# Kernel tuning notes

Measured on AMD Instinct MI355X. Metric: run time of the kernel, lower is better.

The kernel has to match this reference:

```python
import jax, jax.numpy as jnp
import numpy as np
from jax import lax

NUM_GROUP = 512    # G: number of FPS centers
GROUP_SIZE = 32    # M: KNN neighbors per center


def setup_inputs() -> dict:
    key = jax.random.key(0)
    xyz = jax.random.normal(key, (32, 8192, 3), dtype=jnp.float32)  # B N 3
    return {"xyz": xyz}


def _fps(xyz, num_group):
    """Iterative farthest point sampling. xyz: [B,N,3] -> idx [B,G] int32.
    Deterministic start at point 0 (matching pointnet2-style fps)."""
    B, N, _ = xyz.shape

    def step(carry, _):
        dists, last_idx = carry                       # dists: [B,N] running min sq-dist
        last = xyz[jnp.arange(B), last_idx]           # [B,3] most recent center
        d = jnp.sum((xyz - last[:, None, :]) ** 2, axis=-1)  # [B,N]
        dists = jnp.minimum(dists, d)
        nxt = jnp.argmax(dists, axis=-1).astype(jnp.int32)   # farthest point
        return (dists, nxt), nxt

    init_idx = jnp.zeros((B,), jnp.int32)
    init_d = jnp.full((B, N), jnp.inf, xyz.dtype)
    (_, _), idxs = lax.scan(step, (init_d, init_idx), None, length=num_group - 1)
    return jnp.concatenate([init_idx[None, :], idxs], axis=0).T  # [B,G]


def reference(xyz):
    B, N, _ = xyz.shape
    G, M = NUM_GROUP, GROUP_SIZE

    fps_idx = _fps(xyz, G)                              # [B,G] int32
    center = xyz[jnp.arange(B)[:, None], fps_idx]       # [B,G,3]

    # KNN: for each center, k nearest points in xyz (squared euclidean)
    # dist2[b,g,n] = |c|^2 + |x|^2 - 2 c.x   -> [B,G,N]
    x2 = jnp.sum(xyz * xyz, axis=-1)                    # [B,N]
    c2 = jnp.sum(center * center, axis=-1)              # [B,G]
    dist2 = c2[:, :, None] + x2[:, None, :] - 2.0 * jnp.einsum('bgd,bnd->bgn', center, xyz)
    _, idx = lax.top_k(-dist2, M)                       # [B,G,M] nearest-first

    neighborhood = xyz[jnp.arange(B)[:, None, None], idx]   # [B,G,M,3]
    neighborhood = neighborhood - center[:, :, None, :]
    return neighborhood, center, fps_idx
```

## Files before the change

### kernel.cpp

```cpp
#include <hip/hip_runtime.h>
#include <math.h>

#define BATCH  32
#define NPTS   8192
#define NGROUP 512
#define MSIZE  32

#define FPS_THREADS 512
#define SXYZ_FLOATS (NPTS * 3)
#define DYN_LDS_BYTES (SXYZ_FLOATS * 4)

typedef float v2f __attribute__((ext_vector_type(2)));

template<int CTRL>
__device__ __forceinline__ float dpp_max_f32(float x) {
    int o = __builtin_amdgcn_update_dpp(0, __float_as_int(x), CTRL, 0xF, 0xF, true);
    float f = __int_as_float(o);
    return x > f ? x : f;
}
template<int CTRL>
__device__ __forceinline__ unsigned dpp_min_u32_full(unsigned x) {
    unsigned o = (unsigned)__builtin_amdgcn_update_dpp(0, (int)x, CTRL, 0xF, 0xF, true);
    return o < x ? o : x;
}

__global__ __launch_bounds__(FPS_THREADS, 2)
void fps_kernel(const float* __restrict__ xyz,
                float* __restrict__ out_center,
                float* __restrict__ out_fps)
{
#pragma clang fp contract(off)
    extern __shared__ float sxyz[];
    __shared__ unsigned long long gkey[3];

    const int b    = blockIdx.x;
    const int t    = threadIdx.x;
    const int lane = t & 63;
    const float* bp = xyz + (size_t)b * NPTS * 3;
    const float4* bp4 = reinterpret_cast<const float4*>(bp);
    float4* s4 = reinterpret_cast<float4*>(sxyz);

    v2f px2[8], py2[8], pz2[8], dist2[8];
    {
        float f[48];
        #pragma unroll
        for (int q = 0; q < 12; ++q) {
            float4 v = bp4[t * 12 + q];
            s4[t * 12 + q] = v;
            f[q*4+0] = v.x; f[q*4+1] = v.y; f[q*4+2] = v.z; f[q*4+3] = v.w;
        }
        #pragma unroll
        for (int j = 0; j < 8; ++j) {
            px2[j] = (v2f){f[6*j+0], f[6*j+3]};
            py2[j] = (v2f){f[6*j+1], f[6*j+4]};
            pz2[j] = (v2f){f[6*j+2], f[6*j+5]};
            dist2[j] = (v2f){INFINITY, INFINITY};
        }
    }
    if (t == 0) { gkey[0] = 0; gkey[1] = 0; gkey[2] = 0; }
    __syncthreads();

    if (t == 0) {
        out_fps[(size_t)b * NGROUP] = 0.0f;
        out_center[(size_t)(b * NGROUP) * 3 + 0] = sxyz[0];
        out_center[(size_t)(b * NGROUP) * 3 + 1] = sxyz[1];
        out_center[(size_t)(b * NGROUP) * 3 + 2] = sxyz[2];
    }

    int last = 0;
    for (int g = 1; g < NGROUP; ++g) {
        const int slot = g % 3;
        const int nxt  = (g + 1) % 3;
        float lx = sxyz[last*3 + 0];
        float ly = sxyz[last*3 + 1];
        float lz = sxyz[last*3 + 2];

        #pragma unroll
        for (int j = 0; j < 8; ++j) {
            v2f dx = px2[j] - lx;
            v2f dy = py2[j] - ly;
            v2f dz = pz2[j] - lz;
            v2f t1 = dx * dx;
            v2f t2 = dy * dy;
            v2f t3 = dz * dz;
            v2f s  = t1 + t2;
            v2f d  = s + t3;
            dist2[j] = __builtin_elementwise_min(dist2[j], d);
        }
        v2f mm0 = __builtin_elementwise_max(dist2[0], dist2[1]);
        v2f mm1 = __builtin_elementwise_max(dist2[2], dist2[3]);
        v2f mm2 = __builtin_elementwise_max(dist2[4], dist2[5]);
        v2f mm3 = __builtin_elementwise_max(dist2[6], dist2[7]);
        v2f mma = __builtin_elementwise_max(mm0, mm1);
        v2f mmb = __builtin_elementwise_max(mm2, mm3);
        v2f mmc = __builtin_elementwise_max(mma, mmb);
        float m_t = fmaxf(mmc.x, mmc.y);

        float m = m_t;
        m = dpp_max_f32<0xB1>(m);
        m = dpp_max_f32<0x4E>(m);
        m = dpp_max_f32<0x141>(m);
        m = dpp_max_f32<0x140>(m);
        m = dpp_max_f32<0x142>(m);
        m = dpp_max_f32<0x143>(m);
        float wmax = __int_as_float(__builtin_amdgcn_readlane(__float_as_int(m), 63));

        unsigned long long mask = __ballot(m_t == wmax);
        int l = __ffsll((long long)mask) - 1;

        unsigned lj = 0;
        #pragma unroll
        for (int j = 15; j >= 0; --j) {
            float dj = (j & 1) ? dist2[j >> 1].y : dist2[j >> 1].x;
            lj = (dj == wmax) ? (unsigned)j : lj;
        }
        unsigned idx = ((unsigned)t << 4) | lj;
        unsigned widx = (unsigned)__builtin_amdgcn_readlane((int)idx, l);

        if (lane == 63) {
            unsigned long long key =
                (((unsigned long long)__float_as_uint(wmax)) << 32) | (unsigned)~widx;
            atomicMax(&gkey[slot], key);
            if (t == 63) gkey[nxt] = 0;
        }
        __syncthreads();

        unsigned long long kq = gkey[slot];
        int fi = (int)(~(unsigned)kq);
        last = fi;
        if (t == 0) {
            out_fps[(size_t)b * NGROUP + g] = (float)fi;
            out_center[((size_t)(b * NGROUP + g)) * 3 + 0] = sxyz[fi*3 + 0];
            out_center[((size_t)(b * NGROUP + g)) * 3 + 1] = sxyz[fi*3 + 1];
            out_center[((size_t)(b * NGROUP + g)) * 3 + 2] = sxyz[fi*3 + 2];
        }
    }
}

__global__ __launch_bounds__(256)
void knn_kernel(const float* __restrict__ xyz,
                const float* __restrict__ center,
                float* __restrict__ out_nbhd)
{
    const int lane = threadIdx.x & 63;
    const int gid  = blockIdx.x * 4 + (threadIdx.x >> 6);
    const int b    = gid >> 9;
    const float* bp = xyz + (size_t)b * NPTS * 3;
    const float4* bp4 = reinterpret_cast<const float4*>(bp);

    const float cx = center[(size_t)gid*3+0];
    const float cy = center[(size_t)gid*3+1];
    const float cz = center[(size_t)gid*3+2];

    unsigned kl[4];
    #pragma unroll
    for (int k = 0; k < 4; ++k) kl[k] = 0xFFFFFFFFu;

    for (int c = 0; c < 32; ++c) {
        int f4 = c * 192 + lane * 3;
        float4 a  = bp4[f4+0];
        float4 bq = bp4[f4+1];
        float4 cq = bp4[f4+2];
        unsigned p0 = (unsigned)(c * 256 + lane * 4);
        v2f xA = (v2f){a.x,  a.w},  yA = (v2f){a.y,  bq.x}, zA = (v2f){a.z,  bq.y};
        v2f xB = (v2f){bq.z, cq.y}, yB = (v2f){bq.w, cq.z}, zB = (v2f){cq.x, cq.w};
        v2f dxA = xA - cx, dyA = yA - cy, dzA = zA - cz;
        v2f dxB = xB - cx, dyB = yB - cy, dzB = zB - cz;
        v2f dA = dxA*dxA + dyA*dyA + dzA*dzA;
        v2f dB = dxB*dxB + dyB*dyB + dzB*dzB;
        float ds[4] = {dA.x, dA.y, dB.x, dB.y};
        #pragma unroll
        for (int k = 0; k < 4; ++k) {
            unsigned key = (__float_as_uint(ds[k]) & 0xFFFFE000u) | (p0 + k);
            if (key < kl[3]) {
                kl[3] = key;
                #pragma unroll
                for (int q = 3; q > 0; --q) {
                    if (kl[q] < kl[q-1]) {
                        unsigned tk = kl[q]; kl[q] = kl[q-1]; kl[q-1] = tk;
                    }
                }
            }
        }
    }

    int keep = 0;
    #pragma unroll 1
    for (int r = 0; r < MSIZE; ++r) {
        unsigned k = kl[0];
        k = dpp_min_u32_full<0xB1>(k);
        k = dpp_min_u32_full<0x4E>(k);
        k = dpp_min_u32_full<0x141>(k);
        k = dpp_min_u32_full<0x140>(k);
        {
            unsigned o = __shfl_xor(k, 16);
            k = o < k ? o : k;
            o = __shfl_xor(k, 32);
            k = o < k ? o : k;
        }
        if (lane == r) keep = (int)(k & 0x1FFFu);
        if (kl[0] == k) {
            kl[0] = kl[1]; kl[1] = kl[2]; kl[2] = kl[3];
            kl[3] = 0xFFFFFFFFu;
        }
    }

    if (lane < MSIZE) {
        size_t o = ((size_t)gid * MSIZE + lane) * 3;
        float x = bp[keep*3+0], y = bp[keep*3+1], z = bp[keep*3+2];
        out_nbhd[o+0] = x - cx;
        out_nbhd[o+1] = y - cy;
        out_nbhd[o+2] = z - cz;
    }
}

extern "C" void kernel_launch(void* const* d_in, const int* in_sizes, int n_in,
                              void* d_out, int out_size, void* d_ws, size_t ws_size,
                              hipStream_t stream)
{
    const float* xyz = (const float*)d_in[0];
    float* out        = (float*)d_out;
    float* out_nbhd   = out;
    float* out_center = out + (size_t)BATCH*NGROUP*MSIZE*3;
    float* out_fps    = out_center + (size_t)BATCH*NGROUP*3;

    hipFuncSetAttribute(reinterpret_cast<const void*>(fps_kernel),
                        hipFuncAttributeMaxDynamicSharedMemorySize,
                        DYN_LDS_BYTES);

    fps_kernel<<<dim3(BATCH), dim3(FPS_THREADS), DYN_LDS_BYTES, stream>>>(xyz, out_center, out_fps);
    knn_kernel<<<dim3(BATCH*NGROUP/4), dim3(256), 0, stream>>>(xyz, out_center, out_nbhd);
}
```

Before: 577.0 us.

## Stage batch points in LDS as SoA for KNN and drop FPS atomics

The KNN kernel now launches one 512-thread block per batch segment. Each block loads the batch's points into LDS in structure-of-arrays form, and each wavefront handles 8 centers from LDS instead of re-reading global memory. The wave reduction now uses full DPP row broadcasts plus readlane instead of shuffles. In FPS, the per-iteration LDS atomicMax on a rotating slot is replaced by per-wave key writes into a double-buffered array that every thread then reduces, and the per-lane argmax index search becomes a min tree. The KNN grid drops to 256 blocks of 96KB LDS each, which reduces parallelism and may limit latency hiding.

```diff
diff --git a/kernel.cpp b/kernel.cpp
--- a/kernel.cpp
+++ b/kernel.cpp
@@ -9,6 +9,10 @@
 #define FPS_THREADS 512
 #define SXYZ_FLOATS (NPTS * 3)
 #define DYN_LDS_BYTES (SXYZ_FLOATS * 4)
+
+#define KNN_THREADS 512
+#define KNN_SEGS    8
+#define KNN_GPW     8
 
 typedef float v2f __attribute__((ext_vector_type(2)));
 
@@ -22,6 +26,11 @@
 __device__ __forceinline__ unsigned dpp_min_u32_full(unsigned x) {
     unsigned o = (unsigned)__builtin_amdgcn_update_dpp(0, (int)x, CTRL, 0xF, 0xF, true);
     return o < x ? o : x;
+}
+
+__device__ __forceinline__ unsigned long long u64max(unsigned long long a,
+                                                     unsigned long long b) {
+    return a > b ? a : b;
 }
 
 __global__ __launch_bounds__(FPS_THREADS, 2)
@@ -31,11 +40,12 @@
 {
 #pragma clang fp contract(off)
     extern __shared__ float sxyz[];
-    __shared__ unsigned long long gkey[3];
+    __shared__ unsigned long long s_key[2][8];
 
     const int b    = blockIdx.x;
     const int t    = threadIdx.x;
     const int lane = t & 63;
+    const int wid  = t >> 6;
     const float* bp = xyz + (size_t)b * NPTS * 3;
     const float4* bp4 = reinterpret_cast<const float4*>(bp);
     float4* s4 = reinterpret_cast<float4*>(sxyz);
@@ -57,7 +67,6 @@
             dist2[j] = (v2f){INFINITY, INFINITY};
         }
     }
-    if (t == 0) { gkey[0] = 0; gkey[1] = 0; gkey[2] = 0; }
     __syncthreads();
 
     if (t == 0) {
@@ -69,8 +78,6 @@
 
     int last = 0;
     for (int g = 1; g < NGROUP; ++g) {
-        const int slot = g % 3;
-        const int nxt  = (g + 1) % 3;
         float lx = sxyz[last*3 + 0];
         float ly = sxyz[last*3 + 1];
         float lz = sxyz[last*3 + 2];
@@ -108,25 +115,37 @@
         unsigned long long mask = __ballot(m_t == wmax);
         int l = __ffsll((long long)mask) - 1;
 
-        unsigned lj = 0;
-        #pragma unroll
-        for (int j = 15; j >= 0; --j) {
-            float dj = (j & 1) ? dist2[j >> 1].y : dist2[j >> 1].x;
-            lj = (dj == wmax) ? (unsigned)j : lj;
-        }
+        unsigned cand[8];
+        #pragma unroll
+        for (int p = 0; p < 8; ++p) {
+            unsigned c = 0xFFFFFFFFu;
+            c = (dist2[p].y == wmax) ? (unsigned)(2*p + 1) : c;
+            c = (dist2[p].x == wmax) ? (unsigned)(2*p)     : c;
+            cand[p] = c;
+        }
+        unsigned q0 = cand[0] < cand[1] ? cand[0] : cand[1];
+        unsigned q1 = cand[2] < cand[3] ? cand[2] : cand[3];
+        unsigned q2 = cand[4] < cand[5] ? cand[4] : cand[5];
+        unsigned q3 = cand[6] < cand[7] ? cand[6] : cand[7];
+        unsigned qa = q0 < q1 ? q0 : q1;
+        unsigned qb = q2 < q3 ? q2 : q3;
+        unsigned lj = qa < qb ? qa : qb;
         unsigned idx = ((unsigned)t << 4) | lj;
         unsigned widx = (unsigned)__builtin_amdgcn_readlane((int)idx, l);
 
         if (lane == 63) {
-            unsigned long long key =
+            s_key[g & 1][wid] =
                 (((unsigned long long)__float_as_uint(wmax)) << 32) | (unsigned)~widx;
-            atomicMax(&gkey[slot], key);
-            if (t == 63) gkey[nxt] = 0;
         }
         __syncthreads();
 
-        unsigned long long kq = gkey[slot];
-        int fi = (int)(~(unsigned)kq);
+        const unsigned long long* sk = s_key[g & 1];
+        unsigned long long a0 = u64max(sk[0], sk[1]);
+        unsigned long long a1 = u64max(sk[2], sk[3]);
+        unsigned long long a2 = u64max(sk[4], sk[5]);
+        unsigned long long a3 = u64max(sk[6], sk[7]);
+        unsigned long long km = u64max(u64max(a0, a1), u64max(a2, a3));
+        int fi = (int)(~(unsigned)km);
         last = fi;
         if (t == 0) {
             out_fps[(size_t)b * NGROUP + g] = (float)fi;
@@ -137,80 +156,93 @@
     }
 }
 
-__global__ __launch_bounds__(256)
+__global__ __launch_bounds__(KNN_THREADS, 1)
 void knn_kernel(const float* __restrict__ xyz,
                 const float* __restrict__ center,
                 float* __restrict__ out_nbhd)
 {
-    const int lane = threadIdx.x & 63;
-    const int gid  = blockIdx.x * 4 + (threadIdx.x >> 6);
-    const int b    = gid >> 9;
+    extern __shared__ float sm[];
+    float* sx = sm;
+    float* sy = sm + NPTS;
+    float* sz = sm + 2 * NPTS;
+
+    const int t    = threadIdx.x;
+    const int lane = t & 63;
+    const int wid  = t >> 6;
+    const int b    = blockIdx.x >> 3;
+    const int seg  = blockIdx.x & 7;
     const float* bp = xyz + (size_t)b * NPTS * 3;
-    const float4* bp4 = reinterpret_cast<const float4*>(bp);
-
-    const float cx = center[(size_t)gid*3+0];
-    const float cy = center[(size_t)gid*3+1];
-    const float cz = center[(size_t)gid*3+2];
-
-    unsigned kl[4];
+
     #pragma unroll
-    for (int k = 0; k < 4; ++k) kl[k] = 0xFFFFFFFFu;
-
-    for (int c = 0; c < 32; ++c) {
-        int f4 = c * 192 + lane * 3;
-        float4 a  = bp4[f4+0];
-        float4 bq = bp4[f4+1];
-        float4 cq = bp4[f4+2];
-        unsigned p0 = (unsigned)(c * 256 + lane * 4);
-        v2f xA = (v2f){a.x,  a.w},  yA = (v2f){a.y,  bq.x}, zA = (v2f){a.z,  bq.y};
-        v2f xB = (v2f){bq.z, cq.y}, yB = (v2f){bq.w, cq.z}, zB = (v2f){cq.x, cq.w};
-        v2f dxA = xA - cx, dyA = yA - cy, dzA = zA - cz;
-        v2f dxB = xB - cx, dyB = yB - cy, dzB = zB - cz;
-        v2f dA = dxA*dxA + dyA*dyA + dzA*dzA;
-        v2f dB = dxB*dxB + dyB*dyB + dzB*dzB;
-        float ds[4] = {dA.x, dA.y, dB.x, dB.y};
-        #pragma unroll
-        for (int k = 0; k < 4; ++k) {
-            unsigned key = (__float_as_uint(ds[k]) & 0xFFFFE000u) | (p0 + k);
-            if (key < kl[3]) {
-                kl[3] = key;
-                #pragma unroll
-                for (int q = 3; q > 0; --q) {
-                    if (kl[q] < kl[q-1]) {
-                        unsigned tk = kl[q]; kl[q] = kl[q-1]; kl[q-1] = tk;
+    for (int s = 0; s < NPTS / KNN_THREADS; ++s) {
+        const int p = t + KNN_THREADS * s;
+        float3 v = *reinterpret_cast<const float3*>(bp + (size_t)p * 3);
+        sx[p] = v.x; sy[p] = v.y; sz[p] = v.z;
+    }
+    __syncthreads();
+
+    for (int k = 0; k < KNN_GPW; ++k) {
+        const int gid = b * NGROUP + seg * 64 + wid * KNN_GPW + k;
+        const float cx = center[(size_t)gid*3+0];
+        const float cy = center[(size_t)gid*3+1];
+        const float cz = center[(size_t)gid*3+2];
+
+        unsigned kl[4];
+        #pragma unroll
+        for (int q = 0; q < 4; ++q) kl[q] = 0xFFFFFFFFu;
+
+        for (int c = 0; c < 32; ++c) {
+            const int p0i = c * 256 + lane * 4;
+            float4 x4 = *reinterpret_cast<const float4*>(&sx[p0i]);
+            float4 y4 = *reinterpret_cast<const float4*>(&sy[p0i]);
+            float4 z4 = *reinterpret_cast<const float4*>(&sz[p0i]);
+            v2f xA = (v2f){x4.x, x4.y}, yA = (v2f){y4.x, y4.y}, zA = (v2f){z4.x, z4.y};
+            v2f xB = (v2f){x4.z, x4.w}, yB = (v2f){y4.z, y4.w}, zB = (v2f){z4.z, z4.w};
+            v2f dxA = xA - cx, dyA = yA - cy, dzA = zA - cz;
+            v2f dxB = xB - cx, dyB = yB - cy, dzB = zB - cz;
+            v2f dA = dxA*dxA + dyA*dyA + dzA*dzA;
+            v2f dB = dxB*dxB + dyB*dyB + dzB*dzB;
+            float ds[4] = {dA.x, dA.y, dB.x, dB.y};
+            unsigned p0 = (unsigned)p0i;
+            #pragma unroll
+            for (int q = 0; q < 4; ++q) {
+                unsigned key = (__float_as_uint(ds[q]) & 0xFFFFE000u) | (p0 + q);
+                if (key < kl[3]) {
+                    kl[3] = key;
+                    #pragma unroll
+                    for (int w = 3; w > 0; --w) {
+                        if (kl[w] < kl[w-1]) {
+                            unsigned tk = kl[w]; kl[w] = kl[w-1]; kl[w-1] = tk;
+                        }
                     }
                 }
             }
         }
-    }
-
-    int keep = 0;
-    #pragma unroll 1
-    for (int r = 0; r < MSIZE; ++r) {
-        unsigned k = kl[0];
-        k = dpp_min_u32_full<0xB1>(k);
-        k = dpp_min_u32_full<0x4E>(k);
-        k = dpp_min_u32_full<0x141>(k);
-        k = dpp_min_u32_full<0x140>(k);
-        {
-            unsigned o = __shfl_xor(k, 16);
-            k = o < k ? o : k;
-            o = __shfl_xor(k, 32);
-            k = o < k ? o : k;
-        }
-        if (lane == r) keep = (int)(k & 0x1FFFu);
-        if (kl[0] == k) {
-            kl[0] = kl[1]; kl[1] = kl[2]; kl[2] = kl[3];
-            kl[3] = 0xFFFFFFFFu;
-        }
-    }
-
-    if (lane < MSIZE) {
-        size_t o = ((size_t)gid * MSIZE + lane) * 3;
-        float x = bp[keep*3+0], y = bp[keep*3+1], z = bp[keep*3+2];
-        out_nbhd[o+0] = x - cx;
-        out_nbhd[o+1] = y - cy;
-        out_nbhd[o+2] = z - cz;
+
+        int keep = 0;
+        #pragma unroll 1
+        for (int r = 0; r < MSIZE; ++r) {
+            unsigned kk = kl[0];
+            kk = dpp_min_u32_full<0xB1>(kk);
+            kk = dpp_min_u32_full<0x4E>(kk);
+            kk = dpp_min_u32_full<0x141>(kk);
+            kk = dpp_min_u32_full<0x140>(kk);
+            kk = dpp_min_u32_full<0x142>(kk);
+            kk = dpp_min_u32_full<0x143>(kk);
+            unsigned kmin = (unsigned)__builtin_amdgcn_readlane((int)kk, 63);
+            if (lane == r) keep = (int)(kmin & 0x1FFFu);
+            if (kl[0] == kmin) {
+                kl[0] = kl[1]; kl[1] = kl[2]; kl[2] = kl[3];
+                kl[3] = 0xFFFFFFFFu;
+            }
+        }
+
+        if (lane < MSIZE) {
+            size_t o = ((size_t)gid * MSIZE + lane) * 3;
+            out_nbhd[o+0] = sx[keep] - cx;
+            out_nbhd[o+1] = sy[keep] - cy;
+            out_nbhd[o+2] = sz[keep] - cz;
+        }
     }
 }
 
@@ -227,7 +259,10 @@
     hipFuncSetAttribute(reinterpret_cast<const void*>(fps_kernel),
                         hipFuncAttributeMaxDynamicSharedMemorySize,
                         DYN_LDS_BYTES);
+    hipFuncSetAttribute(reinterpret_cast<const void*>(knn_kernel),
+                        hipFuncAttributeMaxDynamicSharedMemorySize,
+                        DYN_LDS_BYTES);
 
     fps_kernel<<<dim3(BATCH), dim3(FPS_THREADS), DYN_LDS_BYTES, stream>>>(xyz, out_center, out_fps);
-    knn_kernel<<<dim3(BATCH*NGROUP/4), dim3(256), 0, stream>>>(xyz, out_center, out_nbhd);
-}
+    knn_kernel<<<dim3(BATCH*KNN_SEGS), dim3(KNN_THREADS), DYN_LDS_BYTES, stream>>>(xyz, out_center, out_nbhd);
+}
```

Result: slower. 818.3 us (+41.8%).

## Fuse FPS and KNN into one cooperative kernel with progress flags

Applied to the files above, without the earlier changes.

Launches one cooperative persistent kernel. Blocks 0-31 run FPS per batch and publish progress counters with release stores every 8 centers. The remaining 224 blocks' waves spin on those counters and run KNN for each center as soon as it is available. The aim is to overlap KNN with the long serial FPS loop instead of running them back to back. The cost is the spin-waiting and the cooperative launch requirement, with a fallback to the two-kernel path if the launch fails or there is no workspace.

```diff
diff --git a/kernel.cpp b/kernel.cpp
--- a/kernel.cpp
+++ b/kernel.cpp
@@ -9,6 +9,12 @@
 #define FPS_THREADS 512
 #define SXYZ_FLOATS (NPTS * 3)
 #define DYN_LDS_BYTES (SXYZ_FLOATS * 4)
+
+#define NBLOCKS      256
+#define WORKER_BLKS  (NBLOCKS - BATCH)
+#define WORKER_WAVES (WORKER_BLKS * 8)
+#define WPB          (WORKER_WAVES / BATCH)
+#define PROG_STRIDE  16
 
 typedef float v2f __attribute__((ext_vector_type(2)));
 
@@ -24,13 +30,13 @@
     return o < x ? o : x;
 }
 
-__global__ __launch_bounds__(FPS_THREADS, 2)
-void fps_kernel(const float* __restrict__ xyz,
-                float* __restrict__ out_center,
-                float* __restrict__ out_fps)
+__device__ __forceinline__ void fps_body(const float* __restrict__ xyz,
+                                         float* __restrict__ out_center,
+                                         float* __restrict__ out_fps,
+                                         unsigned* __restrict__ prog,
+                                         float* sxyz)
 {
 #pragma clang fp contract(off)
-    extern __shared__ float sxyz[];
     __shared__ unsigned long long gkey[3];
 
     const int b    = blockIdx.x;
@@ -62,9 +68,12 @@
 
     if (t == 0) {
         out_fps[(size_t)b * NGROUP] = 0.0f;
-        out_center[(size_t)(b * NGROUP) * 3 + 0] = sxyz[0];
-        out_center[(size_t)(b * NGROUP) * 3 + 1] = sxyz[1];
-        out_center[(size_t)(b * NGROUP) * 3 + 2] = sxyz[2];
+        __hip_atomic_store(&out_center[(size_t)(b*NGROUP)*3 + 0], sxyz[0],
+                           __ATOMIC_RELAXED, __HIP_MEMORY_SCOPE_AGENT);
+        __hip_atomic_store(&out_center[(size_t)(b*NGROUP)*3 + 1], sxyz[1],
+                           __ATOMIC_RELAXED, __HIP_MEMORY_SCOPE_AGENT);
+        __hip_atomic_store(&out_center[(size_t)(b*NGROUP)*3 + 2], sxyz[2],
+                           __ATOMIC_RELAXED, __HIP_MEMORY_SCOPE_AGENT);
     }
 
     int last = 0;
@@ -130,28 +139,26 @@
         last = fi;
         if (t == 0) {
             out_fps[(size_t)b * NGROUP + g] = (float)fi;
-            out_center[((size_t)(b * NGROUP + g)) * 3 + 0] = sxyz[fi*3 + 0];
-            out_center[((size_t)(b * NGROUP + g)) * 3 + 1] = sxyz[fi*3 + 1];
-            out_center[((size_t)(b * NGROUP + g)) * 3 + 2] = sxyz[fi*3 + 2];
-        }
-    }
-}
-
-__global__ __launch_bounds__(256)
-void knn_kernel(const float* __restrict__ xyz,
-                const float* __restrict__ center,
-                float* __restrict__ out_nbhd)
-{
-    const int lane = threadIdx.x & 63;
-    const int gid  = blockIdx.x * 4 + (threadIdx.x >> 6);
-    const int b    = gid >> 9;
-    const float* bp = xyz + (size_t)b * NPTS * 3;
-    const float4* bp4 = reinterpret_cast<const float4*>(bp);
-
-    const float cx = center[(size_t)gid*3+0];
-    const float cy = center[(size_t)gid*3+1];
-    const float cz = center[(size_t)gid*3+2];
-
+            const size_t o3 = ((size_t)(b * NGROUP + g)) * 3;
+            __hip_atomic_store(&out_center[o3 + 0], sxyz[fi*3 + 0],
+                               __ATOMIC_RELAXED, __HIP_MEMORY_SCOPE_AGENT);
+            __hip_atomic_store(&out_center[o3 + 1], sxyz[fi*3 + 1],
+                               __ATOMIC_RELAXED, __HIP_MEMORY_SCOPE_AGENT);
+            __hip_atomic_store(&out_center[o3 + 2], sxyz[fi*3 + 2],
+                               __ATOMIC_RELAXED, __HIP_MEMORY_SCOPE_AGENT);
+            if ((g & 7) == 7)
+                __hip_atomic_store(&prog[b * PROG_STRIDE], (unsigned)(g + 1),
+                                   __ATOMIC_RELEASE, __HIP_MEMORY_SCOPE_AGENT);
+        }
+    }
+}
+
+__device__ __forceinline__ void knn_one_group(const float* __restrict__ bp,
+                                              const float4* __restrict__ bp4,
+                                              int gid, int lane,
+                                              float cx, float cy, float cz,
+                                              float* __restrict__ out_nbhd)
+{
     unsigned kl[4];
     #pragma unroll
     for (int k = 0; k < 4; ++k) kl[k] = 0xFFFFFFFFu;
@@ -214,6 +221,174 @@
     }
 }
 
+__global__ __launch_bounds__(FPS_THREADS, 2)
+void fused_kernel(const float* __restrict__ xyz,
+                  float* __restrict__ out_center,
+                  float* __restrict__ out_fps,
+                  float* __restrict__ out_nbhd,
+                  unsigned* __restrict__ prog)
+{
+    extern __shared__ float sxyz[];
+
+    if (blockIdx.x < BATCH) {
+        fps_body(xyz, out_center, out_fps, prog, sxyz);
+        return;
+    }
+
+    const int t    = threadIdx.x;
+    const int lane = t & 63;
+    const int wid  = t >> 6;
+    const int ww   = (blockIdx.x - BATCH) * 8 + wid;
+    const int b    = ww & 31;
+    const int g0   = ww >> 5;
+    const float* bp = xyz + (size_t)b * NPTS * 3;
+    const float4* bp4 = reinterpret_cast<const float4*>(bp);
+
+    for (int g = g0; g < NGROUP; g += WPB) {
+        while ((int)__hip_atomic_load(&prog[b * PROG_STRIDE],
+                                      __ATOMIC_ACQUIRE, __HIP_MEMORY_SCOPE_AGENT) <= g)
+            __builtin_amdgcn_s_sleep(8);
+
+        const int gid = b * NGROUP + g;
+        float cx = __hip_atomic_load(&out_center[(size_t)gid*3+0],
+                                     __ATOMIC_RELAXED, __HIP_MEMORY_SCOPE_AGENT);
+        float cy = __hip_atomic_load(&out_center[(size_t)gid*3+1],
+                                     __ATOMIC_RELAXED, __HIP_MEMORY_SCOPE_AGENT);
+        float cz = __hip_atomic_load(&out_center[(size_t)gid*3+2],
+                                     __ATOMIC_RELAXED, __HIP_MEMORY_SCOPE_AGENT);
+        knn_one_group(bp, bp4, gid, lane, cx, cy, cz, out_nbhd);
+    }
+}
+
+__global__ __launch_bounds__(FPS_THREADS, 2)
+void fps_kernel(const float* __restrict__ xyz,
+                float* __restrict__ out_center,
+                float* __restrict__ out_fps)
+{
+#pragma clang fp contract(off)
+    extern __shared__ float sxyz[];
+    __shared__ unsigned long long gkey[3];
+
+    const int b    = blockIdx.x;
+    const int t    = threadIdx.x;
+    const int lane = t & 63;
+    const float* bp = xyz + (size_t)b * NPTS * 3;
+    const float4* bp4 = reinterpret_cast<const float4*>(bp);
+    float4* s4 = reinterpret_cast<float4*>(sxyz);
+
+    v2f px2[8], py2[8], pz2[8], dist2[8];
+    {
+        float f[48];
+        #pragma unroll
+        for (int q = 0; q < 12; ++q) {
+            float4 v = bp4[t * 12 + q];
+            s4[t * 12 + q] = v;
+            f[q*4+0] = v.x; f[q*4+1] = v.y; f[q*4+2] = v.z; f[q*4+3] = v.w;
+        }
+        #pragma unroll
+        for (int j = 0; j < 8; ++j) {
+            px2[j] = (v2f){f[6*j+0], f[6*j+3]};
+            py2[j] = (v2f){f[6*j+1], f[6*j+4]};
+            pz2[j] = (v2f){f[6*j+2], f[6*j+5]};
+            dist2[j] = (v2f){INFINITY, INFINITY};
+        }
+    }
+    if (t == 0) { gkey[0] = 0; gkey[1] = 0; gkey[2] = 0; }
+    __syncthreads();
+
+    if (t == 0) {
+        out_fps[(size_t)b * NGROUP] = 0.0f;
+        out_center[(size_t)(b * NGROUP) * 3 + 0] = sxyz[0];
+        out_center[(size_t)(b * NGROUP) * 3 + 1] = sxyz[1];
+        out_center[(size_t)(b * NGROUP) * 3 + 2] = sxyz[2];
+    }
+
+    int last = 0;
+    for (int g = 1; g < NGROUP; ++g) {
+        const int slot = g % 3;
+        const int nxt  = (g + 1) % 3;
+        float lx = sxyz[last*3 + 0];
+        float ly = sxyz[last*3 + 1];
+        float lz = sxyz[last*3 + 2];
+
+        #pragma unroll
+        for (int j = 0; j < 8; ++j) {
+            v2f dx = px2[j] - lx;
+            v2f dy = py2[j] - ly;
+            v2f dz = pz2[j] - lz;
+            v2f t1 = dx * dx;
+            v2f t2 = dy * dy;
+            v2f t3 = dz * dz;
+            v2f s  = t1 + t2;
+            v2f d  = s + t3;
+            dist2[j] = __builtin_elementwise_min(dist2[j], d);
+        }
+        v2f mm0 = __builtin_elementwise_max(dist2[0], dist2[1]);
+        v2f mm1 = __builtin_elementwise_max(dist2[2], dist2[3]);
+        v2f mm2 = __builtin_elementwise_max(dist2[4], dist2[5]);
+        v2f mm3 = __builtin_elementwise_max(dist2[6], dist2[7]);
+        v2f mma = __builtin_elementwise_max(mm0, mm1);
+        v2f mmb = __builtin_elementwise_max(mm2, mm3);
+        v2f mmc = __builtin_elementwise_max(mma, mmb);
+        float m_t = fmaxf(mmc.x, mmc.y);
+
+        float m = m_t;
+        m = dpp_max_f32<0xB1>(m);
+        m = dpp_max_f32<0x4E>(m);
+        m = dpp_max_f32<0x141>(m);
+        m = dpp_max_f32<0x140>(m);
+        m = dpp_max_f32<0x142>(m);
+        m = dpp_max_f32<0x143>(m);
+        float wmax = __int_as_float(__builtin_amdgcn_readlane(__float_as_int(m), 63));
+
+        unsigned long long mask = __ballot(m_t == wmax);
+        int l = __ffsll((long long)mask) - 1;
+
+        unsigned lj = 0;
+        #pragma unroll
+        for (int j = 15; j >= 0; --j) {
+            float dj = (j & 1) ? dist2[j >> 1].y : dist2[j >> 1].x;
+            lj = (dj == wmax) ? (unsigned)j : lj;
+        }
+        unsigned idx = ((unsigned)t << 4) | lj;
+        unsigned widx = (unsigned)__builtin_amdgcn_readlane((int)idx, l);
+
+        if (lane == 63) {
+            unsigned long long key =
+                (((unsigned long long)__float_as_uint(wmax)) << 32) | (unsigned)~widx;
+            atomicMax(&gkey[slot], key);
+            if (t == 63) gkey[nxt] = 0;
+        }
+        __syncthreads();
+
+        unsigned long long kq = gkey[slot];
+        int fi = (int)(~(unsigned)kq);
+        last = fi;
+        if (t == 0) {
+            out_fps[(size_t)b * NGROUP + g] = (float)fi;
+            out_center[((size_t)(b * NGROUP + g)) * 3 + 0] = sxyz[fi*3 + 0];
+            out_center[((size_t)(b * NGROUP + g)) * 3 + 1] = sxyz[fi*3 + 1];
+            out_center[((size_t)(b * NGROUP + g)) * 3 + 2] = sxyz[fi*3 + 2];
+        }
+    }
+}
+
+__global__ __launch_bounds__(256)
+void knn_kernel(const float* __restrict__ xyz,
+                const float* __restrict__ center,
+                float* __restrict__ out_nbhd)
+{
+    const int lane = threadIdx.x & 63;
+    const int gid  = blockIdx.x * 4 + (threadIdx.x >> 6);
+    const int b    = gid >> 9;
+    const float* bp = xyz + (size_t)b * NPTS * 3;
+    const float4* bp4 = reinterpret_cast<const float4*>(bp);
+    const float cx = center[(size_t)gid*3+0];
+    const float cy = center[(size_t)gid*3+1];
+    const float cz = center[(size_t)gid*3+2];
+    knn_one_group(bp, bp4, gid, lane, cx, cy, cz, out_nbhd);
+}
+
 extern "C" void kernel_launch(void* const* d_in, const int* in_sizes, int n_in,
                               void* d_out, int out_size, void* d_ws, size_t ws_size,
                               hipStream_t stream)
@@ -224,10 +399,31 @@
     float* out_center = out + (size_t)BATCH*NGROUP*MSIZE*3;
     float* out_fps    = out_center + (size_t)BATCH*NGROUP*3;
 
+    hipFuncSetAttribute(reinterpret_cast<const void*>(fused_kernel),
+                        hipFuncAttributeMaxDynamicSharedMemorySize,
+                        DYN_LDS_BYTES);
     hipFuncSetAttribute(reinterpret_cast<const void*>(fps_kernel),
                         hipFuncAttributeMaxDynamicSharedMemorySize,
                         DYN_LDS_BYTES);
 
-    fps_kernel<<<dim3(BATCH), dim3(FPS_THREADS), DYN_LDS_BYTES, stream>>>(xyz, out_center, out_fps);
-    knn_kernel<<<dim3(BATCH*NGROUP/4), dim3(256), 0, stream>>>(xyz, out_center, out_nbhd);
-}
+    bool fused_ok = false;
+    if (d_ws != nullptr && ws_size >= (size_t)BATCH * PROG_STRIDE * sizeof(unsigned)) {
+        unsigned* prog = (unsigned*)d_ws;
+        hipMemsetAsync(prog, 0, (size_t)BATCH * PROG_STRIDE * sizeof(unsigned), stream);
+
+        const float* a_xyz = xyz;
+        float* a_oc = out_center; float* a_of = out_fps; float* a_on = out_nbhd;
+        unsigned* a_pr = prog;
+        void* args[5] = {(void*)&a_xyz, (void*)&a_oc, (void*)&a_of,
+                         (void*)&a_on, (void*)&a_pr};
+        hipError_t e = hipLaunchCooperativeKernel(
+            reinterpret_cast<const void*>(fused_kernel),
+            dim3(NBLOCKS), dim3(FPS_THREADS), args, DYN_LDS_BYTES, stream);
+        fused_ok = (e == hipSuccess);
+    }
+
+    if (!fused_ok) {
+        fps_kernel<<<dim3(BATCH), dim3(FPS_THREADS), DYN_LDS_BYTES, stream>>>(xyz, out_center, out_fps);
+        knn_kernel<<<dim3(BATCH*NGROUP/4), dim3(256), 0, stream>>>(xyz, out_center, out_nbhd);
+    }
+}
```

Result: slower. 602.8 us (+4.5%).
